# Performance work log

Measured on AMD Instinct MI355X. Metric: run time of the kernel, lower is better.

Reference implementation:

```python
import jax, jax.numpy as jnp
import numpy as np

N_NODES = 20000
N_GRAPHS = 200
NODES_PER_G = 100
N_EDGES = 100000
D_IN = 64
EMB = 300
N_LAYERS = 5
N_OUT = 10
RATIO = 0.25


def setup_inputs() -> dict:
    key = jax.random.key(0)
    ks = jax.random.split(key, 12)
    rng = np.random.default_rng(0)
    epg = N_EDGES // N_GRAPHS  # edges per graph (equal-sized graphs)
    g_of_e = np.arange(N_EDGES) // epg
    src = rng.integers(0, NODES_PER_G, N_EDGES) + g_of_e * NODES_PER_G
    dst = rng.integers(0, NODES_PER_G, N_EDGES) + g_of_e * NODES_PER_G
    edge_index = jnp.asarray(np.stack([src, dst]), jnp.int32)
    batch_vec = jnp.asarray(np.arange(N_NODES) // NODES_PER_G, jnp.int32)

    def lin(k, fi, fo):
        return jax.random.normal(k, (fi, fo), jnp.float32) / np.sqrt(fi)

    def lin_stack(k, L, fi, fo):
        return jax.random.normal(k, (L, fi, fo), jnp.float32) / np.sqrt(fi)

    return {
        'x': jax.random.normal(ks[0], (N_NODES, D_IN), jnp.float32),
        'edge_index': edge_index,
        'batch_vec': batch_vec,
        'num_graphs': N_GRAPHS,
        'enc_in_W': lin(ks[1], D_IN, EMB), 'enc_in_b': jnp.zeros((EMB,), jnp.float32),
        'enc_W1': lin_stack(ks[2], N_LAYERS, EMB, 2 * EMB), 'enc_b1': jnp.zeros((N_LAYERS, 2 * EMB), jnp.float32),
        'enc_W2': lin_stack(ks[3], N_LAYERS, 2 * EMB, EMB), 'enc_b2': jnp.zeros((N_LAYERS, EMB), jnp.float32),
        'enc_eps': jnp.zeros((N_LAYERS,), jnp.float32),
        'att_W1': lin(ks[4], 2 * EMB, 4 * EMB), 'att_b1': jnp.zeros((4 * EMB,), jnp.float32),
        'att_W2': lin(ks[5], 4 * EMB, 1), 'att_b2': jnp.zeros((1,), jnp.float32),
        'clf_in_W': lin(ks[6], D_IN, EMB), 'clf_in_b': jnp.zeros((EMB,), jnp.float32),
        'clf_W1': lin_stack(ks[7], N_LAYERS, EMB, 2 * EMB), 'clf_b1': jnp.zeros((N_LAYERS, 2 * EMB), jnp.float32),
        'clf_W2': lin_stack(ks[8], N_LAYERS, 2 * EMB, EMB), 'clf_b2': jnp.zeros((N_LAYERS, EMB), jnp.float32),
        'clf_eps': jnp.zeros((N_LAYERS,), jnp.float32),
        'pred_W': lin(ks[9], EMB, N_OUT), 'pred_b': jnp.zeros((N_OUT,), jnp.float32),
    }


def _gin(h, src, dst, W1, b1, W2, b2, eps, n, ew=None):
    # GIN: h' = MLP((1+eps)*h + sum_{j->i} m_j), m_j = h_j * w_e (set_masks edge weighting)
    L = W1.shape[0]
    for l in range(L):
        msg = h[src] if ew is None else h[src] * ew[:, None]
        agg = jax.ops.segment_sum(msg, dst, num_segments=n)
        z = (1.0 + eps[l]) * h + agg
        z = jax.nn.relu(z @ W1[l] + b1[l]) @ W2[l] + b2[l]
        h = jax.nn.relu(z) if l < L - 1 else z
    return h


def reference(x, edge_index, batch_vec, num_graphs, enc_in_W, enc_in_b, enc_W1, enc_b1,
              enc_W2, enc_b2, enc_eps, att_W1, att_b1, att_W2, att_b2, clf_in_W, clf_in_b,
              clf_W1, clf_b1, clf_W2, clf_b2, clf_eps, pred_W, pred_b):
    n = x.shape[0]
    e = edge_index.shape[1]
    src, dst = edge_index[0], edge_index[1]

    # 1) gnn_encoder (GIN, no edge weights)
    h = x @ enc_in_W + enc_in_b
    h = _gin(h, src, dst, enc_W1, enc_b1, enc_W2, enc_b2, enc_eps, n)

    # 2) edge-score MLP on [h_row || h_col]
    edge_rep = jnp.concatenate([h[src], h[dst]], axis=-1)  # [E, 2*EMB]
    score = (jax.nn.relu(edge_rep @ att_W1 + att_b1) @ att_W2 + att_b2).reshape(-1)

    # 3) sparse_topk: segmented descending sort via the argsort trick
    seg = batch_vec[src]  # graph id per edge
    smin, smax = score.min(), score.max()
    norm = (score - smin) / (smax - smin + 1e-12) - seg.astype(score.dtype)
    perm = jnp.argsort(-norm)  # segments ascending, scores descending within segment
    epg = e // num_graphs  # static: equal edges per graph
    K = int(np.ceil(RATIO * epg))
    pos = np.arange(num_graphs)[:, None] * epg + np.arange(K)[None, :]
    causal_idx = perm[jnp.asarray(pos.reshape(-1))]  # topk edges per graph

    c_src, c_dst = src[causal_idx], dst[causal_idx]
    c_w = jax.nn.sigmoid(score[causal_idx])  # set_masks applies sigmoid to the mask

    # 4) relabel-equivalent: classifier on causal subgraph (c_in='raw')
    hc = x @ clf_in_W + clf_in_b
    hc = _gin(hc, c_src, c_dst, clf_W1, clf_b1, clf_W2, clf_b2, clf_eps, n, ew=c_w)

    # mean pooling over nodes touched by causal edges (== relabel node subset)
    mask = jnp.zeros((n,), x.dtype).at[c_src].set(1.0).at[c_dst].set(1.0)
    gsum = jax.ops.segment_sum(hc * mask[:, None], batch_vec, num_segments=num_graphs)
    cnt = jax.ops.segment_sum(mask, batch_vec, num_segments=num_graphs)
    pooled = gsum / jnp.maximum(cnt, 1.0)[:, None]

    return pooled @ pred_W + pred_b  # causal_pred [G, out_dim]
```

## Files before the change

kernel.cpp:

```cpp
#include <hip/hip_runtime.h>
#include <hip/hip_bf16.h>
#include <math.h>

#define N_NODES 20000
#define N_EDGES 100000
#define N_GRAPHS 200
#define NPG 100
#define EPG 500
#define TOPK 125
#define D_IN 64
#define EMB 300
#define H2 600
#define H4 1200
#define NLAYERS 5
#define NOUT 10

#define NPAD 20096
#define EMBP 320
#define H2P 640
#define H4P 1216
#define UVM 2432
#define UVROWS 10112

static inline int cdiv(int a, int b) { return (a + b - 1) / b; }

typedef __attribute__((ext_vector_type(8))) short bfrag;
typedef __attribute__((ext_vector_type(4))) float f32x4;

__device__ __forceinline__ ushort f2bf(float f) {
    unsigned u = __builtin_bit_cast(unsigned, f);
    unsigned r = u + 0x7FFFu + ((u >> 16) & 1u);
    return (ushort)(r >> 16);
}
__device__ __forceinline__ float bf2f(ushort h) {
    unsigned u = ((unsigned)h) << 16;
    return __builtin_bit_cast(float, u);
}

template<int NT>
__device__ __forceinline__ void split_planes(float v, ushort& p0, ushort& p1, ushort& p2) {
    p0 = f2bf(v);
    float r = v - bf2f(p0);
    p1 = f2bf(r);
    if (NT == 3) { r -= bf2f(p1); p2 = f2bf(r); } else { p2 = 0; }
}

#define GLOAD_LDS16(gsrc, ldst)                                                   \
    __builtin_amdgcn_global_load_lds(                                             \
        (const __attribute__((address_space(1))) void*)(gsrc),                    \
        (__attribute__((address_space(3))) void*)(ldst), 16, 0, 0)

template<int NT, int RELU, int EPI, int BN>
__launch_bounds__(256)
__global__ void mfma_gemm(const ushort* __restrict__ A0, const ushort* __restrict__ A1,
                          const ushort* __restrict__ A2,
                          const ushort* __restrict__ B0, const ushort* __restrict__ B1,
                          const ushort* __restrict__ B2,
                          const float* __restrict__ bias, int Kp, int Mvalid, int ldc,
                          float* __restrict__ Cf, ushort* __restrict__ C0,
                          ushort* __restrict__ C1, ushort* __restrict__ C2) {
    constexpr int NCOL   = BN / 32;
    constexpr int ABYTES = 8192;
    constexpr int BBYTES = BN * 64;
    __shared__ char smem[NT * ABYTES + NT * BBYTES];
    const int tid = threadIdx.x;
    const int wave = tid >> 6, lane = tid & 63;
    const int wr = wave >> 1, wc = wave & 1;

    int bx, by;
    {
        const int gx = gridDim.x;
        const int nwg = gx * gridDim.y;
        const int wg = blockIdx.y * gx + blockIdx.x;
        const int q = nwg >> 3, rch = nwg & 7;
        const int xc = wg & 7, k = wg >> 3;
        const int virt = (xc < rch ? xc * (q + 1) : rch * (q + 1) + (xc - rch) * q) + k;
        bx = virt % gx;
        by = virt / gx;
    }
    const long rowbase = (long)by * 128;
    const int n0 = bx * BN;

    const ushort* Ap[3] = {A0, A1, A2};
    const ushort* Bp[3] = {B0, B1, B2};

    f32x4 acc[4][NCOL] = {};

    const int arow0 = wave * 16 + (lane >> 2);
    const int aq = lane & 3;

    for (int k0 = 0; k0 < Kp; k0 += 32) {
#pragma unroll
        for (int p = 0; p < NT; ++p) {
            {
                int r = arow0;
                int q = aq ^ ((r >> 1) & 3);
                GLOAD_LDS16(Ap[p] + (size_t)(rowbase + r) * Kp + k0 + q * 8,
                            smem + p * ABYTES + wave * 1024);
            }
            {
                int r = arow0 + 64;
                int q = aq ^ ((r >> 1) & 3);
                GLOAD_LDS16(Ap[p] + (size_t)(rowbase + r) * Kp + k0 + q * 8,
                            smem + p * ABYTES + 4096 + wave * 1024);
            }
            {
                int r = arow0;
                int q = aq ^ ((r >> 1) & 3);
                GLOAD_LDS16(Bp[p] + (size_t)(n0 + r) * Kp + k0 + q * 8,
                            smem + NT * ABYTES + p * BBYTES + wave * 1024);
            }
            if (BN == 128) {
                int r = arow0 + 64;
                int q = aq ^ ((r >> 1) & 3);
                GLOAD_LDS16(Bp[p] + (size_t)(n0 + r) * Kp + k0 + q * 8,
                            smem + NT * ABYTES + p * BBYTES + 4096 + wave * 1024);
            }
        }
        __syncthreads();

        bfrag bfr[NCOL][3];
#pragma unroll
        for (int n = 0; n < NCOL; ++n)
#pragma unroll
            for (int p = 0; p < NT; ++p) {
                int rB = wc * (BN / 2) + n * 16 + (lane & 15);
                int q = (lane >> 4) ^ ((rB >> 1) & 3);
                bfr[n][p] = *(const bfrag*)(smem + NT * ABYTES + p * BBYTES + rB * 64 + q * 16);
            }
#pragma unroll
        for (int m = 0; m < 4; ++m) {
            bfrag afr[3];
#pragma unroll
            for (int p = 0; p < NT; ++p) {
                int rA = wr * 64 + m * 16 + (lane & 15);
                int q = (lane >> 4) ^ ((rA >> 1) & 3);
                afr[p] = *(const bfrag*)(smem + p * ABYTES + rA * 64 + q * 16);
            }
#pragma unroll
            for (int n = 0; n < NCOL; ++n) {
#pragma unroll
                for (int pa = 0; pa < NT; ++pa)
#pragma unroll
                    for (int pb = 0; pb < NT; ++pb)
                        if (pa + pb <= NT - 1)
                            acc[m][n] = __builtin_amdgcn_mfma_f32_16x16x32_bf16(
                                afr[pa], bfr[n][pb], acc[m][n], 0, 0, 0);
            }
        }
        __syncthreads();
    }

    const int colc = lane & 15, rquad = lane >> 4;
#pragma unroll
    for (int m = 0; m < 4; ++m) {
#pragma unroll
        for (int n = 0; n < NCOL; ++n) {
            long grow0 = rowbase + wr * 64 + m * 16 + rquad * 4;
            int gcol = n0 + wc * (BN / 2) + n * 16 + colc;
            bool cvld = gcol < Mvalid;
            float bv = (bias != nullptr && cvld) ? bias[gcol] : 0.f;
#pragma unroll
            for (int e = 0; e < 4; ++e) {
                float v = acc[m][n][e] + bv;
                if (RELU) v = fmaxf(v, 0.f);
                if (!cvld) v = 0.f;
                size_t o = (size_t)(grow0 + e) * ldc + gcol;
                if (EPI == 0) {
                    Cf[o] = v;
                } else {
                    ushort p0, p1, p2;
                    split_planes<NT>(v, p0, p1, p2);
                    C0[o] = p0; C1[o] = p1;
                    if (NT == 3) C2[o] = p2;
                }
            }
        }
    }
}

template<int NT>
__global__ void conv_w(const float* __restrict__ W, int K, int M, int Kp, int Mp,
                       ushort* __restrict__ P0, ushort* __restrict__ P1,
                       ushort* __restrict__ P2) {
    int idx = blockIdx.x * 256 + threadIdx.x;
    if (idx >= Mp * Kp) return;
    int m = idx / Kp, k = idx % Kp;
    float v = (m < M && k < K) ? W[(size_t)k * M + m] : 0.f;
    ushort p0, p1, p2;
    split_planes<NT>(v, p0, p1, p2);
    P0[idx] = p0; P1[idx] = p1;
    if (NT == 3) P2[idx] = p2;
}

template<int NT>
__global__ void conv_w2(const float* __restrict__ Wa, const float* __restrict__ Wb,
                        ushort* __restrict__ A0, ushort* __restrict__ A1,
                        ushort* __restrict__ A2, ushort* __restrict__ B0,
                        ushort* __restrict__ B1, ushort* __restrict__ B2) {
    int idx = blockIdx.x * 256 + threadIdx.x;
    const int T1 = H2P * EMBP;
    if (idx < T1) {
        int m = idx / EMBP, k = idx % EMBP;
        float v = (m < H2 && k < EMB) ? Wa[(size_t)k * H2 + m] : 0.f;
        ushort p0, p1, p2;
        split_planes<NT>(v, p0, p1, p2);
        A0[idx] = p0; A1[idx] = p1;
        if (NT == 3) A2[idx] = p2;
    } else if (idx < 2 * T1) {
        idx -= T1;
        int m = idx / H2P, k = idx % H2P;
        float v = (m < EMB && k < H2) ? Wb[(size_t)k * EMB + m] : 0.f;
        ushort p0, p1, p2;
        split_planes<NT>(v, p0, p1, p2);
        B0[idx] = p0; B1[idx] = p1;
        if (NT == 3) B2[idx] = p2;
    }
}

template<int NT>
__global__ void conv_a(const float* __restrict__ X, int rows_valid, int ldx, int Kv, int Kp,
                       ushort* __restrict__ P0, ushort* __restrict__ P1,
                       ushort* __restrict__ P2, long total) {
    long idx = (long)blockIdx.x * 256 + threadIdx.x;
    if (idx >= total) return;
    int r = (int)(idx / Kp), k = (int)(idx % Kp);
    float v = (r < rows_valid && k < Kv) ? X[(size_t)r * ldx + k] : 0.f;
    ushort p0, p1, p2;
    split_planes<NT>(v, p0, p1, p2);
    P0[idx] = p0; P1[idx] = p1;
    if (NT == 3) P2[idx] = p2;
}

__global__ void build_At(const int* __restrict__ src, const int* __restrict__ dst,
                         const float* __restrict__ w, float* __restrict__ At, int E) {
    int e = blockIdx.x * 256 + threadIdx.x;
    if (e >= E) return;
    int s = src[e], d = dst[e];
    int g = s / NPG;
    atomicAdd(&At[(size_t)g * NPG * NPG + (size_t)(s - g * NPG) * NPG + (d - g * NPG)],
              w ? w[e] : 1.f);
}

template<int NT, int ROWS>
__device__ __forceinline__ void agg_rows(const float* __restrict__ hg,
                                         const float* __restrict__ Ag,
                                         int rb, int c, bool cv, float ep, int g,
                                         ushort* __restrict__ z0,
                                         ushort* __restrict__ z1,
                                         ushort* __restrict__ z2) {
    float acc[ROWS];
#pragma unroll
    for (int r = 0; r < ROWS; ++r) acc[r] = 0.f;
#pragma unroll 4
    for (int k = 0; k < NPG; ++k) {
        float hv = cv ? hg[k * EMBP + c] : 0.f;
        const float* ak = Ag + k * NPG + rb;
#pragma unroll
        for (int r = 0; r < ROWS; ++r) acc[r] += ak[r] * hv;
    }
#pragma unroll
    for (int r = 0; r < ROWS; ++r) {
        int row = g * NPG + rb + r;
        float z = cv ? acc[r] + ep * hg[(rb + r) * EMBP + c] : 0.f;
        ushort p0, p1, p2;
        split_planes<NT>(z, p0, p1, p2);
        size_t o = (size_t)row * EMBP + c;
        z0[o] = p0; z1[o] = p1;
        if (NT == 3) z2[o] = p2;
    }
}

template<int NT>
__launch_bounds__(512)
__global__ void agg_gemm(const float* __restrict__ h, const float* __restrict__ At,
                         const float* __restrict__ eps, int l,
                         ushort* __restrict__ z0, ushort* __restrict__ z1,
                         ushort* __restrict__ z2) {
    int g = blockIdx.x;
    int strip = blockIdx.y;
    int lane = threadIdx.x & 63;
    int wave = threadIdx.x >> 6;
    int rb = __builtin_amdgcn_readfirstlane(wave * 13);
    const float* Ag = At + (size_t)g * NPG * NPG;
    const float* hg = h + (size_t)g * NPG * EMBP;
    float ep = 1.f + eps[l];

    int c = strip * 64 + lane;
    bool cv = c < EMB;

    if (wave < 7)
        agg_rows<NT, 13>(hg, Ag, rb, c, cv, ep, g, z0, z1, z2);
    else
        agg_rows<NT, 9>(hg, Ag, rb, c, cv, ep, g, z0, z1, z2);
}

__global__ void edge_score(const float* __restrict__ uv, const float* __restrict__ b1,
                           const float* __restrict__ W2, const float* __restrict__ b2,
                           const int* __restrict__ src, const int* __restrict__ dst,
                           float* __restrict__ score, int E, int node_base) {
    int e = blockIdx.x * 4 + (threadIdx.x >> 6);
    int lane = threadIdx.x & 63;
    if (e >= E) return;
    const float* up = uv + (size_t)(src[e] - node_base) * UVM;
    const float* vp = uv + (size_t)(dst[e] - node_base) * UVM + 1216;
    float acc = 0.f;
    for (int j = lane; j < H4; j += 64) {
        float hj = fmaxf(up[j] + vp[j] + b1[j], 0.f);
        acc += hj * W2[j];
    }
#pragma unroll
    for (int o = 32; o > 0; o >>= 1) acc += __shfl_down(acc, o, 64);
    if (lane == 0) score[e] = acc + b2[0];
}

__global__ void topk_kernel(const float* __restrict__ score, const int* __restrict__ src,
                            const int* __restrict__ dst, int* __restrict__ c_src,
                            int* __restrict__ c_dst, float* __restrict__ c_w,
                            float* __restrict__ mask) {
    __shared__ float s[512];
    __shared__ short sidx[512];
    int g = blockIdx.x, t = threadIdx.x;
    int base = g * EPG;
    s[t] = (t < EPG) ? score[base + t] : -1e30f;
    sidx[t] = (short)t;
    __syncthreads();
    for (int k = 2; k <= 512; k <<= 1) {
        for (int j = k >> 1; j > 0; j >>= 1) {
            int ixj = t ^ j;
            if (ixj > t) {
                float a = s[t], b = s[ixj];
                bool desc = ((t & k) == 0);
                if (desc ? (a < b) : (a > b)) {
                    s[t] = b; s[ixj] = a;
                    short tmp = sidx[t]; sidx[t] = sidx[ixj]; sidx[ixj] = tmp;
                }
            }
            __syncthreads();
        }
    }
    if (t < TOPK) {
        int e = base + sidx[t];
        int sn = src[e], dn = dst[e];
        c_src[g * TOPK + t] = sn;
        c_dst[g * TOPK + t] = dn;
        c_w[g * TOPK + t] = 1.f / (1.f + expf(-s[t]));
        mask[sn] = 1.f;
        mask[dn] = 1.f;
    }
}

__global__ void pool_pred(const float* __restrict__ hc, const float* __restrict__ mask,
                          const float* __restrict__ W, const float* __restrict__ b,
                          float* __restrict__ out) {
    int g = blockIdx.x, t = threadIdx.x;
    __shared__ float mloc[NPG];
    __shared__ float pooled[EMB];
    __shared__ float cnt;
    if (t < NPG) mloc[t] = mask[g * NPG + t];
    __syncthreads();
    if (t == 0) {
        float c = 0.f;
        for (int n = 0; n < NPG; ++n) c += mloc[n];
        cnt = fmaxf(c, 1.f);
    }
    __syncthreads();
    for (int c0 = t; c0 < EMB; c0 += 256) {
        float acc = 0.f;
        for (int n = 0; n < NPG; ++n)
            acc += mloc[n] * hc[((size_t)g * NPG + n) * EMBP + c0];
        pooled[c0] = acc / cnt;
    }
    __syncthreads();
    if (t < NOUT) {
        float acc = b[t];
        for (int c0 = 0; c0 < EMB; ++c0) acc += pooled[c0] * W[c0 * NOUT + t];
        out[g * NOUT + t] = acc;
    }
}

extern "C" void kernel_launch(void* const* d_in, const int* in_sizes, int n_in,
                              void* d_out, int out_size, void* d_ws, size_t ws_size,
                              hipStream_t stream) {
    const float* x        = (const float*)d_in[0];
    const int*   eidx     = (const int*)d_in[1];
    const float* enc_in_W = (const float*)d_in[4];
    const float* enc_in_b = (const float*)d_in[5];
    const float* enc_W1   = (const float*)d_in[6];
    const float* enc_b1   = (const float*)d_in[7];
    const float* enc_W2   = (const float*)d_in[8];
    const float* enc_b2   = (const float*)d_in[9];
    const float* enc_eps  = (const float*)d_in[10];
    const float* att_W1   = (const float*)d_in[11];
    const float* att_b1   = (const float*)d_in[12];
    const float* att_W2   = (const float*)d_in[13];
    const float* att_b2   = (const float*)d_in[14];
    const float* clf_in_W = (const float*)d_in[15];
    const float* clf_in_b = (const float*)d_in[16];
    const float* clf_W1   = (const float*)d_in[17];
    const float* clf_b1   = (const float*)d_in[18];
    const float* clf_W2   = (const float*)d_in[19];
    const float* clf_b2   = (const float*)d_in[20];
    const float* clf_eps  = (const float*)d_in[21];
    const float* pred_W   = (const float*)d_in[22];
    const float* pred_b   = (const float*)d_in[23];
    float* out = (float*)d_out;

    const int* src = eidx;
    const int* dst = eidx + N_EDGES;

    char* ws = (char*)d_ws;
    constexpr size_t SZ_H    = (size_t)NPAD * EMBP * 4;
    constexpr size_t SZ_ZP   = (size_t)NPAD * EMBP * 2;
    constexpr size_t SZ_TP   = (size_t)NPAD * H2P * 2;
    constexpr size_t SZ_WSP  = (size_t)H2P * EMBP * 2;
    constexpr size_t SZ_WUVP = (size_t)UVM * EMBP * 2;

    constexpr size_t OFF_H   = 0;
    constexpr size_t OFF_Z   = OFF_H + SZ_H;
    constexpr size_t OFF_T   = OFF_Z + 3 * SZ_ZP;
    constexpr size_t OFF_WSL = OFF_T + 3 * SZ_TP;
    constexpr size_t OFF_AT  = OFF_WSL + 6 * SZ_WSP;
    constexpr size_t OFF_SC  = OFF_AT + (size_t)N_GRAPHS * NPG * NPG * 4;
    constexpr size_t OFF_CW  = OFF_SC + (size_t)N_EDGES * 4;
    constexpr size_t OFF_MK  = OFF_CW + (size_t)N_GRAPHS * TOPK * 4;
    constexpr size_t OFF_CS  = OFF_MK + (size_t)N_NODES * 4;
    constexpr size_t OFF_CD  = OFF_CS + (size_t)N_GRAPHS * TOPK * 4;
    constexpr size_t OFF_UV  = OFF_CD + (size_t)N_GRAPHS * TOPK * 4;

    float*  h   = (float*)(ws + OFF_H);
    ushort* z0  = (ushort*)(ws + OFF_Z);
    ushort* z1  = (ushort*)(ws + OFF_Z + SZ_ZP);
    ushort* z2  = (ushort*)(ws + OFF_Z + 2 * SZ_ZP);
    ushort* t0  = (ushort*)(ws + OFF_T);
    ushort* t1  = (ushort*)(ws + OFF_T + SZ_TP);
    ushort* t2  = (ushort*)(ws + OFF_T + 2 * SZ_TP);
    ushort* w0p[3] = {(ushort*)(ws + OFF_WSL), (ushort*)(ws + OFF_WSL + SZ_WSP),
                      (ushort*)(ws + OFF_WSL + 2 * SZ_WSP)};
    ushort* w1p[3] = {(ushort*)(ws + OFF_WSL + 3 * SZ_WSP), (ushort*)(ws + OFF_WSL + 4 * SZ_WSP),
                      (ushort*)(ws + OFF_WSL + 5 * SZ_WSP)};
    float*  At    = (float*)(ws + OFF_AT);
    float*  score = (float*)(ws + OFF_SC);
    float*  c_w   = (float*)(ws + OFF_CW);
    float*  mask  = (float*)(ws + OFF_MK);
    int*    c_src = (int*)(ws + OFF_CS);
    int*    c_dst = (int*)(ws + OFF_CD);
    float*  uvbuf = (float*)(ws + OFF_UV);

    ushort* xp[3] = {z0, z1, z2};
    ushort* wuvp[3] = {(ushort*)(ws + OFF_T), (ushort*)(ws + OFF_T + SZ_WUVP),
                       (ushort*)(ws + OFF_T + 2 * SZ_WUVP)};

    conv_w<3><<<(EMBP * 64) / 256, 256, 0, stream>>>(enc_in_W, D_IN, EMB, 64, EMBP,
                                                     w0p[0], w0p[1], w0p[2]);
    conv_a<3><<<(int)(((long)NPAD * 64) / 256), 256, 0, stream>>>(
        x, N_NODES, D_IN, D_IN, 64, xp[0], xp[1], xp[2], (long)NPAD * 64);
    mfma_gemm<3, 0, 0, 64><<<dim3(EMBP / 64, NPAD / 128), 256, 0, stream>>>(
        xp[0], xp[1], xp[2], w0p[0], w0p[1], w0p[2], enc_in_b, 64, EMB, EMBP,
        h, nullptr, nullptr, nullptr);

    hipMemsetAsync(At, 0, (size_t)N_GRAPHS * NPG * NPG * 4, stream);
    build_At<<<cdiv(N_EDGES, 256), 256, 0, stream>>>(src, dst, nullptr, At, N_EDGES);

    for (int l = 0; l < NLAYERS; ++l) {
        agg_gemm<3><<<dim3(N_GRAPHS, 5), 512, 0, stream>>>(h, At, enc_eps, l, z0, z1, z2);
        conv_w2<3><<<(2 * H2P * EMBP) / 256, 256, 0, stream>>>(
            enc_W1 + (size_t)l * EMB * H2, enc_W2 + (size_t)l * H2 * EMB,
            w0p[0], w0p[1], w0p[2], w1p[0], w1p[1], w1p[2]);
        mfma_gemm<3, 1, 1, 128><<<dim3(H2P / 128, NPAD / 128), 256, 0, stream>>>(
            z0, z1, z2, w0p[0], w0p[1], w0p[2], enc_b1 + l * H2, EMBP, H2, H2P,
            nullptr, t0, t1, t2);
        if (l < NLAYERS - 1)
            mfma_gemm<3, 1, 0, 64><<<dim3(EMBP / 64, NPAD / 128), 256, 0, stream>>>(
                t0, t1, t2, w1p[0], w1p[1], w1p[2], enc_b2 + l * EMB, H2P, EMB, EMBP,
                h, nullptr, nullptr, nullptr);
        else
            mfma_gemm<3, 0, 1, 64><<<dim3(EMBP / 64, NPAD / 128), 256, 0, stream>>>(
                t0, t1, t2, w1p[0], w1p[1], w1p[2], enc_b2 + l * EMB, H2P, EMB, EMBP,
                nullptr, z0, z1, z2);
    }

    conv_w<3><<<cdiv(1216 * EMBP, 256), 256, 0, stream>>>(
        att_W1, EMB, H4, EMBP, 1216, wuvp[0], wuvp[1], wuvp[2]);
    conv_w<3><<<cdiv(1216 * EMBP, 256), 256, 0, stream>>>(
        att_W1 + (size_t)EMB * H4, EMB, H4, EMBP, 1216,
        wuvp[0] + (size_t)1216 * EMBP, wuvp[1] + (size_t)1216 * EMBP,
        wuvp[2] + (size_t)1216 * EMBP);
    for (int sc = 0; sc < 2; ++sc) {
        size_t nb0 = (size_t)sc * 10000;
        mfma_gemm<3, 0, 0, 128><<<dim3(UVM / 128, UVROWS / 128), 256, 0, stream>>>(
            z0 + nb0 * EMBP, z1 + nb0 * EMBP, z2 + nb0 * EMBP,
            wuvp[0], wuvp[1], wuvp[2], nullptr, EMBP, UVM, UVM,
            uvbuf, nullptr, nullptr, nullptr);
        edge_score<<<cdiv(N_EDGES / 2, 4), 256, 0, stream>>>(
            uvbuf, att_b1, att_W2, att_b2, src + sc * 50000, dst + sc * 50000,
            score + sc * 50000, N_EDGES / 2, (int)nb0);
    }
    hipMemsetAsync(mask, 0, N_NODES * 4, stream);
    topk_kernel<<<N_GRAPHS, 512, 0, stream>>>(score, src, dst, c_src, c_dst, c_w, mask);

    conv_w<2><<<(EMBP * 64) / 256, 256, 0, stream>>>(clf_in_W, D_IN, EMB, 64, EMBP,
                                                     w0p[0], w0p[1], w0p[2]);
    conv_a<2><<<(int)(((long)NPAD * 64) / 256), 256, 0, stream>>>(
        x, N_NODES, D_IN, D_IN, 64, xp[0], xp[1], nullptr, (long)NPAD * 64);
    mfma_gemm<2, 0, 0, 64><<<dim3(EMBP / 64, NPAD / 128), 256, 0, stream>>>(
        xp[0], xp[1], nullptr, w0p[0], w0p[1], nullptr, clf_in_b, 64, EMB, EMBP,
        h, nullptr, nullptr, nullptr);

    hipMemsetAsync(At, 0, (size_t)N_GRAPHS * NPG * NPG * 4, stream);
    build_At<<<cdiv(N_GRAPHS * TOPK, 256), 256, 0, stream>>>(c_src, c_dst, c_w, At,
                                                             N_GRAPHS * TOPK);

    for (int l = 0; l < NLAYERS; ++l) {
        agg_gemm<2><<<dim3(N_GRAPHS, 5), 512, 0, stream>>>(h, At, clf_eps, l,
                                                           z0, z1, nullptr);
        conv_w2<2><<<(2 * H2P * EMBP) / 256, 256, 0, stream>>>(
            clf_W1 + (size_t)l * EMB * H2, clf_W2 + (size_t)l * H2 * EMB,
            w0p[0], w0p[1], nullptr, w1p[0], w1p[1], nullptr);
        mfma_gemm<2, 1, 1, 128><<<dim3(H2P / 128, NPAD / 128), 256, 0, stream>>>(
            z0, z1, nullptr, w0p[0], w0p[1], nullptr, clf_b1 + l * H2, EMBP, H2, H2P,
            nullptr, t0, t1, nullptr);
        if (l < NLAYERS - 1)
            mfma_gemm<2, 1, 0, 64><<<dim3(EMBP / 64, NPAD / 128), 256, 0, stream>>>(
                t0, t1, nullptr, w1p[0], w1p[1], nullptr, clf_b2 + l * EMB, H2P, EMB, EMBP,
                h, nullptr, nullptr, nullptr);
        else
            mfma_gemm<2, 0, 0, 64><<<dim3(EMBP / 64, NPAD / 128), 256, 0, stream>>>(
                t0, t1, nullptr, w1p[0], w1p[1], nullptr, clf_b2 + l * EMB, H2P, EMB, EMBP,
                h, nullptr, nullptr, nullptr);
    }

    pool_pred<<<N_GRAPHS, 256, 0, stream>>>(h, mask, pred_W, pred_b, out);
}
```

Measured before the change: 1.900 ms.

## Batch per-layer weight conversions into single launches and vectorize aggregation columns

All five layers' MLP weights are now split into bf16 planes by one conv_stack launch into a dedicated workspace region, replacing the per-layer conv_w2 launches. The two att_W1 half conversions are merged into one conv_uv launch. The aggregation kernel now processes two columns per lane with float2 loads and ushort2 stores for the first 256 columns, cutting its grid from 5 to 3 strips. The goal is fewer small launches and better memory vectorization, at the cost of a larger workspace at a hardcoded offset.

```diff
diff --git a/kernel.cpp b/kernel.cpp
--- a/kernel.cpp
+++ b/kernel.cpp
@@ -21,6 +21,7 @@
 #define H4P 1216
 #define UVM 2432
 #define UVROWS 10112
+#define T1W (H2P * EMBP)
 
 static inline int cdiv(int a, int b) { return (a + b - 1) / b; }
 
@@ -194,28 +195,42 @@
 }
 
 template<int NT>
-__global__ void conv_w2(const float* __restrict__ Wa, const float* __restrict__ Wb,
-                        ushort* __restrict__ A0, ushort* __restrict__ A1,
-                        ushort* __restrict__ A2, ushort* __restrict__ B0,
-                        ushort* __restrict__ B1, ushort* __restrict__ B2) {
+__global__ void conv_stack(const float* __restrict__ W1s, const float* __restrict__ W2s,
+                           ushort* __restrict__ wall) {
     int idx = blockIdx.x * 256 + threadIdx.x;
-    const int T1 = H2P * EMBP;
-    if (idx < T1) {
-        int m = idx / EMBP, k = idx % EMBP;
-        float v = (m < H2 && k < EMB) ? Wa[(size_t)k * H2 + m] : 0.f;
-        ushort p0, p1, p2;
-        split_planes<NT>(v, p0, p1, p2);
-        A0[idx] = p0; A1[idx] = p1;
-        if (NT == 3) A2[idx] = p2;
-    } else if (idx < 2 * T1) {
-        idx -= T1;
-        int m = idx / H2P, k = idx % H2P;
-        float v = (m < EMB && k < H2) ? Wb[(size_t)k * EMB + m] : 0.f;
-        ushort p0, p1, p2;
-        split_planes<NT>(v, p0, p1, p2);
-        B0[idx] = p0; B1[idx] = p1;
-        if (NT == 3) B2[idx] = p2;
-    }
+    const int TOT = NLAYERS * 2 * T1W;
+    if (idx >= TOT) return;
+    int half = idx / (NLAYERS * T1W);
+    int r = idx - half * (NLAYERS * T1W);
+    int l = r / T1W, e = r - l * T1W;
+    float v;
+    if (half == 0) {
+        int m = e / EMBP, k = e - m * EMBP;
+        v = (m < H2 && k < EMB) ? W1s[(size_t)l * EMB * H2 + (size_t)k * H2 + m] : 0.f;
+    } else {
+        int m = e / H2P, k = e - m * H2P;
+        v = (m < EMB && k < H2) ? W2s[(size_t)l * H2 * EMB + (size_t)k * EMB + m] : 0.f;
+    }
+    ushort p0, p1, p2;
+    split_planes<NT>(v, p0, p1, p2);
+    size_t base = (size_t)l * (2 * NT * T1W) + (size_t)half * (NT * T1W) + e;
+    wall[base] = p0;
+    wall[base + T1W] = p1;
+    if (NT == 3) wall[base + 2 * T1W] = p2;
+}
+
+__global__ void conv_uv(const float* __restrict__ W, ushort* __restrict__ P0,
+                        ushort* __restrict__ P1, ushort* __restrict__ P2) {
+    int idx = blockIdx.x * 256 + threadIdx.x;
+    if (idx >= UVM * EMBP) return;
+    int m = idx / EMBP, k = idx - m * EMBP;
+    int half = m >= 1216;
+    int mm = m - (half ? 1216 : 0);
+    float v = (mm < H4 && k < EMB)
+                  ? W[((size_t)k + (half ? EMB : 0)) * H4 + mm] : 0.f;
+    ushort p0, p1, p2;
+    split_planes<3>(v, p0, p1, p2);
+    P0[idx] = p0; P1[idx] = p1; P2[idx] = p2;
 }
 
 template<int NT>
@@ -242,32 +257,52 @@
               w ? w[e] : 1.f);
 }
 
-template<int NT, int ROWS>
+template<int NT, int ROWS, int VW>
 __device__ __forceinline__ void agg_rows(const float* __restrict__ hg,
                                          const float* __restrict__ Ag,
-                                         int rb, int c, bool cv, float ep, int g,
+                                         int rb, int c0, float ep, int g,
                                          ushort* __restrict__ z0,
                                          ushort* __restrict__ z1,
                                          ushort* __restrict__ z2) {
-    float acc[ROWS];
-#pragma unroll
-    for (int r = 0; r < ROWS; ++r) acc[r] = 0.f;
+    float acc[ROWS][VW];
+#pragma unroll
+    for (int r = 0; r < ROWS; ++r)
+#pragma unroll
+        for (int w = 0; w < VW; ++w) acc[r][w] = 0.f;
+    const bool cv = (VW == 2) ? true : (c0 < EMB);
 #pragma unroll 4
     for (int k = 0; k < NPG; ++k) {
-        float hv = cv ? hg[k * EMBP + c] : 0.f;
+        float hv[VW];
+        if (VW == 2) {
+            float2 t = *(const float2*)(hg + (size_t)k * EMBP + c0);
+            hv[0] = t.x; hv[1] = t.y;
+        } else {
+            hv[0] = cv ? hg[(size_t)k * EMBP + c0] : 0.f;
+        }
         const float* ak = Ag + k * NPG + rb;
 #pragma unroll
-        for (int r = 0; r < ROWS; ++r) acc[r] += ak[r] * hv;
+        for (int r = 0; r < ROWS; ++r)
+#pragma unroll
+            for (int w = 0; w < VW; ++w) acc[r][w] += ak[r] * hv[w];
     }
 #pragma unroll
     for (int r = 0; r < ROWS; ++r) {
         int row = g * NPG + rb + r;
-        float z = cv ? acc[r] + ep * hg[(rb + r) * EMBP + c] : 0.f;
-        ushort p0, p1, p2;
-        split_planes<NT>(z, p0, p1, p2);
-        size_t o = (size_t)row * EMBP + c;
-        z0[o] = p0; z1[o] = p1;
-        if (NT == 3) z2[o] = p2;
+        size_t o = (size_t)row * EMBP + c0;
+        ushort p0[VW], p1[VW], p2[VW];
+#pragma unroll
+        for (int w = 0; w < VW; ++w) {
+            float z = cv ? acc[r][w] + ep * hg[(size_t)(rb + r) * EMBP + c0 + w] : 0.f;
+            split_planes<NT>(z, p0[w], p1[w], p2[w]);
+        }
+        if (VW == 2) {
+            ushort2 t0v; t0v.x = p0[0]; t0v.y = p0[1]; *(ushort2*)(z0 + o) = t0v;
+            ushort2 t1v; t1v.x = p1[0]; t1v.y = p1[1]; *(ushort2*)(z1 + o) = t1v;
+            if (NT == 3) { ushort2 t2v; t2v.x = p2[0]; t2v.y = p2[1]; *(ushort2*)(z2 + o) = t2v; }
+        } else {
+            z0[o] = p0[0]; z1[o] = p1[0];
+            if (NT == 3) z2[o] = p2[0];
+        }
     }
 }
 
@@ -286,13 +321,15 @@
     const float* hg = h + (size_t)g * NPG * EMBP;
     float ep = 1.f + eps[l];
 
-    int c = strip * 64 + lane;
-    bool cv = c < EMB;
-
-    if (wave < 7)
-        agg_rows<NT, 13>(hg, Ag, rb, c, cv, ep, g, z0, z1, z2);
-    else
-        agg_rows<NT, 9>(hg, Ag, rb, c, cv, ep, g, z0, z1, z2);
+    if (strip < 2) {
+        int c0 = strip * 128 + lane * 2;
+        if (wave < 7) agg_rows<NT, 13, 2>(hg, Ag, rb, c0, ep, g, z0, z1, z2);
+        else          agg_rows<NT, 9, 2>(hg, Ag, rb, c0, ep, g, z0, z1, z2);
+    } else {
+        int c0 = 256 + lane;
+        if (wave < 7) agg_rows<NT, 13, 1>(hg, Ag, rb, c0, ep, g, z0, z1, z2);
+        else          agg_rows<NT, 9, 1>(hg, Ag, rb, c0, ep, g, z0, z1, z2);
+    }
 }
 
 __global__ void edge_score(const float* __restrict__ uv, const float* __restrict__ b1,
@@ -427,6 +464,7 @@
     constexpr size_t OFF_CS  = OFF_MK + (size_t)N_NODES * 4;
     constexpr size_t OFF_CD  = OFF_CS + (size_t)N_GRAPHS * TOPK * 4;
     constexpr size_t OFF_UV  = OFF_CD + (size_t)N_GRAPHS * TOPK * 4;
+    constexpr size_t OFF_WALL = 251083008;
 
     float*  h   = (float*)(ws + OFF_H);
     ushort* z0  = (ushort*)(ws + OFF_Z);
@@ -437,8 +475,6 @@
     ushort* t2  = (ushort*)(ws + OFF_T + 2 * SZ_TP);
     ushort* w0p[3] = {(ushort*)(ws + OFF_WSL), (ushort*)(ws + OFF_WSL + SZ_WSP),
                       (ushort*)(ws + OFF_WSL + 2 * SZ_WSP)};
-    ushort* w1p[3] = {(ushort*)(ws + OFF_WSL + 3 * SZ_WSP), (ushort*)(ws + OFF_WSL + 4 * SZ_WSP),
-                      (ushort*)(ws + OFF_WSL + 5 * SZ_WSP)};
     float*  At    = (float*)(ws + OFF_AT);
     float*  score = (float*)(ws + OFF_SC);
     float*  c_w   = (float*)(ws + OFF_CW);
@@ -446,6 +482,7 @@
     int*    c_src = (int*)(ws + OFF_CS);
     int*    c_dst = (int*)(ws + OFF_CD);
     float*  uvbuf = (float*)(ws + OFF_UV);
+    ushort* wall  = (ushort*)(ws + OFF_WALL);
 
     ushort* xp[3] = {z0, z1, z2};
     ushort* wuvp[3] = {(ushort*)(ws + OFF_T), (ushort*)(ws + OFF_T + SZ_WUVP),
@@ -455,6 +492,7 @@
                                                      w0p[0], w0p[1], w0p[2]);
     conv_a<3><<<(int)(((long)NPAD * 64) / 256), 256, 0, stream>>>(
         x, N_NODES, D_IN, D_IN, 64, xp[0], xp[1], xp[2], (long)NPAD * 64);
+    conv_stack<3><<<cdiv(NLAYERS * 2 * T1W, 256), 256, 0, stream>>>(enc_W1, enc_W2, wall);
     mfma_gemm<3, 0, 0, 64><<<dim3(EMBP / 64, NPAD / 128), 256, 0, stream>>>(
         xp[0], xp[1], xp[2], w0p[0], w0p[1], w0p[2], enc_in_b, 64, EMB, EMBP,
         h, nullptr, nullptr, nullptr);
@@ -463,29 +501,22 @@
     build_At<<<cdiv(N_EDGES, 256), 256, 0, stream>>>(src, dst, nullptr, At, N_EDGES);
 
     for (int l = 0; l < NLAYERS; ++l) {
-        agg_gemm<3><<<dim3(N_GRAPHS, 5), 512, 0, stream>>>(h, At, enc_eps, l, z0, z1, z2);
-        conv_w2<3><<<(2 * H2P * EMBP) / 256, 256, 0, stream>>>(
-            enc_W1 + (size_t)l * EMB * H2, enc_W2 + (size_t)l * H2 * EMB,
-            w0p[0], w0p[1], w0p[2], w1p[0], w1p[1], w1p[2]);
+        ushort* wl = wall + (size_t)l * 6 * T1W;
+        agg_gemm<3><<<dim3(N_GRAPHS, 3), 512, 0, stream>>>(h, At, enc_eps, l, z0, z1, z2);
         mfma_gemm<3, 1, 1, 128><<<dim3(H2P / 128, NPAD / 128), 256, 0, stream>>>(
-            z0, z1, z2, w0p[0], w0p[1], w0p[2], enc_b1 + l * H2, EMBP, H2, H2P,
+            z0, z1, z2, wl, wl + T1W, wl + 2 * T1W, enc_b1 + l * H2, EMBP, H2, H2P,
             nullptr, t0, t1, t2);
         if (l < NLAYERS - 1)
             mfma_gemm<3, 1, 0, 64><<<dim3(EMBP / 64, NPAD / 128), 256, 0, stream>>>(
-                t0, t1, t2, w1p[0], w1p[1], w1p[2], enc_b2 + l * EMB, H2P, EMB, EMBP,
-                h, nullptr, nullptr, nullptr);
+                t0, t1, t2, wl + 3 * T1W, wl + 4 * T1W, wl + 5 * T1W,
+                enc_b2 + l * EMB, H2P, EMB, EMBP, h, nullptr, nullptr, nullptr);
         else
             mfma_gemm<3, 0, 1, 64><<<dim3(EMBP / 64, NPAD / 128), 256, 0, stream>>>(
-                t0, t1, t2, w1p[0], w1p[1], w1p[2], enc_b2 + l * EMB, H2P, EMB, EMBP,
-                nullptr, z0, z1, z2);
-    }
-
-    conv_w<3><<<cdiv(1216 * EMBP, 256), 256, 0, stream>>>(
-        att_W1, EMB, H4, EMBP, 1216, wuvp[0], wuvp[1], wuvp[2]);
-    conv_w<3><<<cdiv(1216 * EMBP, 256), 256, 0, stream>>>(
-        att_W1 + (size_t)EMB * H4, EMB, H4, EMBP, 1216,
-        wuvp[0] + (size_t)1216 * EMBP, wuvp[1] + (size_t)1216 * EMBP,
-        wuvp[2] + (size_t)1216 * EMBP);
+                t0, t1, t2, wl + 3 * T1W, wl + 4 * T1W, wl + 5 * T1W,
+                enc_b2 + l * EMB, H2P, EMB, EMBP, nullptr, z0, z1, z2);
+    }
+
+    conv_uv<<<cdiv(UVM * EMBP, 256), 256, 0, stream>>>(att_W1, wuvp[0], wuvp[1], wuvp[2]);
     for (int sc = 0; sc < 2; ++sc) {
         size_t nb0 = (size_t)sc * 10000;
         mfma_gemm<3, 0, 0, 128><<<dim3(UVM / 128, UVROWS / 128), 256, 0, stream>>>(
@@ -503,6 +534,7 @@
                                                      w0p[0], w0p[1], w0p[2]);
     conv_a<2><<<(int)(((long)NPAD * 64) / 256), 256, 0, stream>>>(
         x, N_NODES, D_IN, D_IN, 64, xp[0], xp[1], nullptr, (long)NPAD * 64);
+    conv_stack<2><<<cdiv(NLAYERS * 2 * T1W, 256), 256, 0, stream>>>(clf_W1, clf_W2, wall);
     mfma_gemm<2, 0, 0, 64><<<dim3(EMBP / 64, NPAD / 128), 256, 0, stream>>>(
         xp[0], xp[1], nullptr, w0p[0], w0p[1], nullptr, clf_in_b, 64, EMB, EMBP,
         h, nullptr, nullptr, nullptr);
@@ -512,22 +544,20 @@
                                                              N_GRAPHS * TOPK);
 
     for (int l = 0; l < NLAYERS; ++l) {
-        agg_gemm<2><<<dim3(N_GRAPHS, 5), 512, 0, stream>>>(h, At, clf_eps, l,
+        ushort* wl = wall + (size_t)l * 4 * T1W;
+        agg_gemm<2><<<dim3(N_GRAPHS, 3), 512, 0, stream>>>(h, At, clf_eps, l,
                                                            z0, z1, nullptr);
-        conv_w2<2><<<(2 * H2P * EMBP) / 256, 256, 0, stream>>>(
-            clf_W1 + (size_t)l * EMB * H2, clf_W2 + (size_t)l * H2 * EMB,
-            w0p[0], w0p[1], nullptr, w1p[0], w1p[1], nullptr);
         mfma_gemm<2, 1, 1, 128><<<dim3(H2P / 128, NPAD / 128), 256, 0, stream>>>(
-            z0, z1, nullptr, w0p[0], w0p[1], nullptr, clf_b1 + l * H2, EMBP, H2, H2P,
+            z0, z1, nullptr, wl, wl + T1W, nullptr, clf_b1 + l * H2, EMBP, H2, H2P,
             nullptr, t0, t1, nullptr);
         if (l < NLAYERS - 1)
             mfma_gemm<2, 1, 0, 64><<<dim3(EMBP / 64, NPAD / 128), 256, 0, stream>>>(
-                t0, t1, nullptr, w1p[0], w1p[1], nullptr, clf_b2 + l * EMB, H2P, EMB, EMBP,
-                h, nullptr, nullptr, nullptr);
+                t0, t1, nullptr, wl + 2 * T1W, wl + 3 * T1W, nullptr,
+                clf_b2 + l * EMB, H2P, EMB, EMBP, h, nullptr, nullptr, nullptr);
         else
             mfma_gemm<2, 0, 0, 64><<<dim3(EMBP / 64, NPAD / 128), 256, 0, stream>>>(
-                t0, t1, nullptr, w1p[0], w1p[1], nullptr, clf_b2 + l * EMB, H2P, EMB, EMBP,
-                h, nullptr, nullptr, nullptr);
+                t0, t1, nullptr, wl + 2 * T1W, wl + 3 * T1W, nullptr,
+                clf_b2 + l * EMB, H2P, EMB, EMBP, h, nullptr, nullptr, nullptr);
     }
 
     pool_pred<<<N_GRAPHS, 256, 0, stream>>>(h, mask, pred_W, pred_b, out);
```

Measured after the change: 1.865 ms. Within noise of the previous version (-1.8%).
